# Kernel tuning notes

Hardware: AMD Instinct MI355X
Metric: run time of the kernel (lower is better)

## Reference

```python
import jax, jax.numpy as jnp
import numpy as np

B, W, C, H = 2, 2048, 1024, 16
K = C // H  # 64
LN_EPS = 1e-5


def setup_inputs() -> dict:
    key = jax.random.key(0)
    ks = jax.random.split(key, 8)
    return {
        "seq1": jax.random.normal(ks[0], (B, W, C), jnp.float32),
        "seq2": jax.random.normal(ks[1], (B, W, C), jnp.float32),
        "ln_gamma": jnp.ones((C,), jnp.float32),
        "ln_beta": jnp.zeros((C,), jnp.float32),
        "q_proj": jax.random.normal(ks[2], (H, C, K), jnp.float32) * 0.02,
        "k_proj": jax.random.normal(ks[3], (H, C, K), jnp.float32) * 0.02,
        "v_proj": jax.random.normal(ks[4], (H, C, K), jnp.float32) * 0.02,
        "mixer_w": jax.random.normal(ks[5], (C, C), jnp.float32) * 0.02,
        "mixer_b": jnp.zeros((C,), jnp.float32),
    }


def _layernorm(x, gamma, beta):
    mu = jnp.mean(x, axis=-1, keepdims=True)
    var = jnp.mean(jnp.square(x - mu), axis=-1, keepdims=True)
    return (x - mu) * jax.lax.rsqrt(var + LN_EPS) * gamma + beta


def reference(seq1, seq2, ln_gamma, ln_beta, q_proj, k_proj, v_proj, mixer_w, mixer_b):
    x1 = _layernorm(seq1, ln_gamma, ln_beta)  # [B,W,C]
    x2 = _layernorm(seq2, ln_gamma, ln_beta)
    # per-head projections: [B,W,C] x [H,C,K] -> [B,H,W,K]
    q = jnp.einsum("bwc,hck->bhwk", x1, q_proj)
    k = jnp.einsum("bwc,hck->bhwk", x2, k_proj)
    v = jnp.einsum("bwc,hck->bhwk", x2, v_proj)
    scores = jnp.einsum("bhqk,bhmk->bhqm", q, k) / jnp.sqrt(jnp.float32(K))
    # causal mask (is_decoder=True)
    causal = jnp.tril(jnp.ones((W, W), bool))
    scores = jnp.where(causal[None, None], scores, jnp.float32(-jnp.inf))
    probs = jax.nn.softmax(scores, axis=-1)
    out = jnp.einsum("bhqm,bhmk->bhqk", probs, v)  # [B,H,W,K]
    out = out.transpose(0, 2, 1, 3).reshape(B, W, C)  # [B,W,C]
    return out @ mixer_w.T + mixer_b
```

## Files before the change

### kernel.cpp

```cpp
#include <hip/hip_runtime.h>
#include <math.h>

#define B_ 2
#define W_ 2048
#define C_ 1024
#define H_ 16
#define K_ 64
#define LN_EPS 1e-5f

typedef __attribute__((ext_vector_type(8))) short short8;
typedef __attribute__((ext_vector_type(4))) float float4v;

#if __has_builtin(__builtin_amdgcn_exp2f)
#define EXP2(x) __builtin_amdgcn_exp2f(x)
#else
#define EXP2(x) exp2f(x)
#endif

__device__ inline unsigned short f2bf(float f) {
  unsigned u = __float_as_uint(f);
  u += 0x7fffu + ((u >> 16) & 1u);
  return (unsigned short)(u >> 16);
}

__device__ inline float max3f(float a, float b, float c) {
  return fmaxf(fmaxf(a, b), c);
}

__device__ __forceinline__ void gload_lds16(const short* g, short* l) {
  __builtin_amdgcn_global_load_lds(
      (const __attribute__((address_space(1))) void*)g,
      (__attribute__((address_space(3))) void*)l, 16, 0, 0);
}

__device__ inline float block_sum(float val) {
  __shared__ float sb[4];
  #pragma unroll
  for (int o = 32; o > 0; o >>= 1) val += __shfl_down(val, o, 64);
  int lane = threadIdx.x & 63, wid = threadIdx.x >> 6;
  if (lane == 0) sb[wid] = val;
  __syncthreads();
  float r = sb[0] + sb[1] + sb[2] + sb[3];
  __syncthreads();
  return r;
}

__global__ __launch_bounds__(256) void ln_kernel(
    const float* __restrict__ seq1, const float* __restrict__ seq2,
    const float* __restrict__ gamma, const float* __restrict__ beta,
    short* __restrict__ x1b, short* __restrict__ x2b) {
  int row = blockIdx.x;
  const int nrows = B_ * W_;
  bool first = row < nrows;
  const float* src = first ? seq1 : seq2;
  short* dst = first ? x1b : x2b;
  int r = first ? row : row - nrows;

  const float4* p = (const float4*)(src + (size_t)r * C_);
  float4 v = p[threadIdx.x];
  float mean = block_sum(v.x + v.y + v.z + v.w) * (1.0f / C_);
  float dx = v.x - mean, dy = v.y - mean, dz = v.z - mean, dw = v.w - mean;
  float var = block_sum(dx * dx + dy * dy + dz * dz + dw * dw) * (1.0f / C_);
  float rstd = rsqrtf(var + LN_EPS);

  float4 g = ((const float4*)gamma)[threadIdx.x];
  float4 b = ((const float4*)beta)[threadIdx.x];
  uint2 o;
  o.x = (unsigned)f2bf(dx * rstd * g.x + b.x) |
        ((unsigned)f2bf(dy * rstd * g.y + b.y) << 16);
  o.y = (unsigned)f2bf(dz * rstd * g.z + b.z) |
        ((unsigned)f2bf(dw * rstd * g.w + b.w) << 16);
  ((uint2*)(dst + (size_t)r * C_))[threadIdx.x] = o;
}

__global__ __launch_bounds__(256) void wprep_proj_kernel(
    const float* __restrict__ qp, const float* __restrict__ kp,
    const float* __restrict__ vp,
    short* __restrict__ wqt, short* __restrict__ wkt, short* __restrict__ wvt) {
  int cb = blockIdx.x, h = blockIdx.y, which = blockIdx.z;
  const float* P = (which == 0 ? qp : (which == 1 ? kp : vp)) + (size_t)h * C_ * K_;
  short* Wt = (which == 0 ? wqt : (which == 1 ? wkt : wvt));
  float scale = (which == 0) ? 0.125f * 1.4426950408889634f : 1.0f;

  __shared__ float Ls[64][65];
  int t = threadIdx.x;
  {
    int cr = t >> 2, ks = (t & 3) * 16;
    const float* src = P + (size_t)(cb * 64 + cr) * K_ + ks;
    #pragma unroll
    for (int j = 0; j < 4; ++j) {
      float4 v = *(const float4*)(src + j * 4);
      Ls[cr][ks + j * 4 + 0] = v.x; Ls[cr][ks + j * 4 + 1] = v.y;
      Ls[cr][ks + j * 4 + 2] = v.z; Ls[cr][ks + j * 4 + 3] = v.w;
    }
  }
  __syncthreads();
  int kr = t >> 2, cs = (t & 3) * 16;
  unsigned u[8];
  #pragma unroll
  for (int i = 0; i < 8; ++i) {
    float a = Ls[cs + 2 * i][kr] * scale;
    float b = Ls[cs + 2 * i + 1][kr] * scale;
    u[i] = (unsigned)f2bf(a) | ((unsigned)f2bf(b) << 16);
  }
  short* dst = Wt + ((size_t)h * 64 + kr) * C_ + cb * 64 + cs;
  uint4 p0; p0.x = u[0]; p0.y = u[1]; p0.z = u[2]; p0.w = u[3];
  uint4 p1; p1.x = u[4]; p1.y = u[5]; p1.z = u[6]; p1.w = u[7];
  *(uint4*)dst = p0;
  *(uint4*)(dst + 8) = p1;
}

__global__ __launch_bounds__(256) void wprep_mix_kernel(
    const float* __restrict__ wm, short* __restrict__ wmb) {
  int gid = blockIdx.x * 256 + threadIdx.x;
  float4 v = ((const float4*)wm)[gid];
  uint2 o;
  o.x = (unsigned)f2bf(v.x) | ((unsigned)f2bf(v.y) << 16);
  o.y = (unsigned)f2bf(v.z) | ((unsigned)f2bf(v.w) << 16);
  ((uint2*)wmb)[gid] = o;
}

__device__ __forceinline__ void gemm_core(
    const short* __restrict__ A, const short* __restrict__ Bt,
    int arow0, int brow0, short* As, short* Bs, float4v acc[4][4]) {
  int tid = threadIdx.x;
  int wave = tid >> 6, lane = tid & 63;
  int lr = lane >> 3, lc = lane & 7;
  int sc = lc ^ lr;
  int wr = wave >> 1, wc = wave & 1;
  int lg = lane >> 4, ll = lane & 15;

  #pragma unroll
  for (int mi = 0; mi < 4; ++mi)
    #pragma unroll
    for (int ni = 0; ni < 4; ++ni) {
      acc[mi][ni][0] = 0.f; acc[mi][ni][1] = 0.f;
      acc[mi][ni][2] = 0.f; acc[mi][ni][3] = 0.f;
    }

  for (int k0 = 0; k0 < C_; k0 += 64) {
    __syncthreads();
    #pragma unroll
    for (int j = 0; j < 4; ++j) {
      int seg = wave * 4 + j;
      int r = seg * 8 + lr;
      gload_lds16(A + (size_t)(arow0 + r) * C_ + k0 + sc * 8, As + seg * 512);
      gload_lds16(Bt + (size_t)(brow0 + r) * C_ + k0 + sc * 8, Bs + seg * 512);
    }
    __syncthreads();
    #pragma unroll
    for (int kc = 0; kc < 2; ++kc) {
      int cc = kc * 4 + lg;
      short8 af[4], bf[4];
      #pragma unroll
      for (int mi = 0; mi < 4; ++mi) {
        int m = wr * 64 + mi * 16 + ll;
        af[mi] = *(const short8*)&As[m * 64 + ((cc ^ (m & 7)) << 3)];
      }
      #pragma unroll
      for (int ni = 0; ni < 4; ++ni) {
        int n = wc * 64 + ni * 16 + ll;
        bf[ni] = *(const short8*)&Bs[n * 64 + ((cc ^ (n & 7)) << 3)];
      }
      #pragma unroll
      for (int mi = 0; mi < 4; ++mi)
        #pragma unroll
        for (int ni = 0; ni < 4; ++ni)
          acc[mi][ni] = __builtin_amdgcn_mfma_f32_16x16x32_bf16(
              af[mi], bf[ni], acc[mi][ni], 0, 0, 0);
    }
  }
}

__device__ __forceinline__ void gemm_core64(
    const short* __restrict__ A, const short* __restrict__ Bt,
    int arow0, int brow0, short* As, short* Bs, float4v acc[2][4]) {
  int tid = threadIdx.x;
  int wave = tid >> 6, lane = tid & 63;
  int lr = lane >> 3, lc = lane & 7;
  int sc = lc ^ lr;
  int wr = wave >> 1, wc = wave & 1;
  int lg = lane >> 4, ll = lane & 15;

  #pragma unroll
  for (int mi = 0; mi < 2; ++mi)
    #pragma unroll
    for (int ni = 0; ni < 4; ++ni) {
      acc[mi][ni][0] = 0.f; acc[mi][ni][1] = 0.f;
      acc[mi][ni][2] = 0.f; acc[mi][ni][3] = 0.f;
    }

  for (int k0 = 0; k0 < C_; k0 += 64) {
    __syncthreads();
    #pragma unroll
    for (int j = 0; j < 2; ++j) {
      int seg = wave * 2 + j;
      int r = seg * 8 + lr;
      gload_lds16(A + (size_t)(arow0 + r) * C_ + k0 + sc * 8, As + seg * 512);
    }
    #pragma unroll
    for (int j = 0; j < 4; ++j) {
      int seg = wave * 4 + j;
      int r = seg * 8 + lr;
      gload_lds16(Bt + (size_t)(brow0 + r) * C_ + k0 + sc * 8, Bs + seg * 512);
    }
    __syncthreads();
    #pragma unroll
    for (int kc = 0; kc < 2; ++kc) {
      int cc = kc * 4 + lg;
      short8 af[2], bf[4];
      #pragma unroll
      for (int mi = 0; mi < 2; ++mi) {
        int m = wr * 32 + mi * 16 + ll;
        af[mi] = *(const short8*)&As[m * 64 + ((cc ^ (m & 7)) << 3)];
      }
      #pragma unroll
      for (int ni = 0; ni < 4; ++ni) {
        int n = wc * 64 + ni * 16 + ll;
        bf[ni] = *(const short8*)&Bs[n * 64 + ((cc ^ (n & 7)) << 3)];
      }
      #pragma unroll
      for (int mi = 0; mi < 2; ++mi)
        #pragma unroll
        for (int ni = 0; ni < 4; ++ni)
          acc[mi][ni] = __builtin_amdgcn_mfma_f32_16x16x32_bf16(
              af[mi], bf[ni], acc[mi][ni], 0, 0, 0);
    }
  }
}

__global__ __launch_bounds__(256, 3) void gemm_qkv_kernel(
    const short* __restrict__ x1b, const short* __restrict__ x2b,
    const short* __restrict__ wqt, const short* __restrict__ wkt,
    const short* __restrict__ wvt,
    short* __restrict__ qb, short* __restrict__ kb, short* __restrict__ vtb) {
  __shared__ short As[128 * 64], Bs[128 * 64];
  int z = blockIdx.z;
  const short *A, *Bt;
  int arow0, brow0;
  if (z == 0)      { A = x1b; Bt = wqt; arow0 = blockIdx.x * 128; brow0 = blockIdx.y * 128; }
  else if (z == 1) { A = x2b; Bt = wkt; arow0 = blockIdx.x * 128; brow0 = blockIdx.y * 128; }
  else             { A = wvt; Bt = x2b; arow0 = blockIdx.y * 128; brow0 = blockIdx.x * 128; }

  float4v acc[4][4];
  gemm_core(A, Bt, arow0, brow0, As, Bs, acc);

  int wave = threadIdx.x >> 6, lane = threadIdx.x & 63;
  int wr = wave >> 1, wc = wave & 1, lg = lane >> 4, ll = lane & 15;
  if (z <= 1) {
    short* O = (z == 0) ? qb : kb;
    #pragma unroll
    for (int mi = 0; mi < 4; ++mi)
      #pragma unroll
      for (int ni = 0; ni < 4; ++ni) {
        int n = brow0 + wc * 64 + ni * 16 + ll;
        int h = n >> 6, kk = n & 63;
        #pragma unroll
        for (int r2 = 0; r2 < 4; ++r2) {
          int m = arow0 + wr * 64 + mi * 16 + lg * 4 + r2;
          int b = m >> 11, w = m & (W_ - 1);
          O[((size_t)(b * H_ + h) * W_ + w) * K_ + kk] = (short)f2bf(acc[mi][ni][r2]);
        }
      }
  } else {
    #pragma unroll
    for (int mi = 0; mi < 4; ++mi)
      #pragma unroll
      for (int ni = 0; ni < 4; ++ni) {
        int n = brow0 + wc * 64 + ni * 16 + ll;
        int b = n >> 11, w = n & (W_ - 1);
        #pragma unroll
        for (int r2 = 0; r2 < 4; ++r2) {
          int m = arow0 + wr * 64 + mi * 16 + lg * 4 + r2;
          int h = m >> 6, kk = m & 63;
          vtb[((size_t)(b * H_ + h) * K_ + kk) * W_ + w] = (short)f2bf(acc[mi][ni][r2]);
        }
      }
  }
}

__global__ __launch_bounds__(256, 3) void gemm_mix_kernel(
    const short* __restrict__ attnb, const short* __restrict__ wmb,
    const float* __restrict__ bias, float* __restrict__ out) {
  __shared__ short As[64 * 64], Bs[128 * 64];
  int arow0 = blockIdx.x * 64, brow0 = blockIdx.y * 128;
  float4v acc[2][4];
  gemm_core64(attnb, wmb, arow0, brow0, As, Bs, acc);

  int wave = threadIdx.x >> 6, lane = threadIdx.x & 63;
  int wr = wave >> 1, wc = wave & 1, lg = lane >> 4, ll = lane & 15;
  #pragma unroll
  for (int mi = 0; mi < 2; ++mi)
    #pragma unroll
    for (int ni = 0; ni < 4; ++ni) {
      int n = brow0 + wc * 64 + ni * 16 + ll;
      float bv = bias[n];
      #pragma unroll
      for (int r2 = 0; r2 < 4; ++r2) {
        int m = arow0 + wr * 32 + mi * 16 + lg * 4 + r2;
        out[(size_t)m * C_ + n] = acc[mi][ni][r2] + bv;
      }
    }
}

__global__ __launch_bounds__(256, 3) void attn_mfma_kernel(
    const short* __restrict__ q, const short* __restrict__ k,
    const short* __restrict__ vt, short* __restrict__ out) {
  int bh = blockIdx.x;
  int b = bh >> 4, h = bh & 15;
  int s = blockIdx.y;
  int qt = (s < 16) ? (31 - s) : (s - 16);
  int wave = threadIdx.x >> 6;
  int lane = threadIdx.x & 63;
  int lg = lane >> 4, ll = lane & 15;

  __shared__ short Ks[2][64 * 64];
  __shared__ short Vs[2][64 * 64];
  __shared__ short Ps[4][16 * 72];

  const short* qp = q + (size_t)bh * W_ * K_;
  const short* kp = k + (size_t)bh * W_ * K_;
  const short* vb = vt + (size_t)bh * K_ * W_;

  int qrow = qt * 64 + wave * 16 + ll;
  short8 aq[2];
  #pragma unroll
  for (int kc = 0; kc < 2; ++kc)
    aq[kc] = *(const short8*)(qp + (size_t)qrow * K_ + kc * 32 + lg * 8);

  short8 ones;
  #pragma unroll
  for (int i = 0; i < 8; ++i) ones[i] = (short)0x3F80;

  float4v o[4];
  #pragma unroll
  for (int ct = 0; ct < 4; ++ct) {
    o[ct][0] = 0.f; o[ct][1] = 0.f; o[ct][2] = 0.f; o[ct][3] = 0.f;
  }
  float4v lsum;
  lsum[0] = 0.f; lsum[1] = 0.f; lsum[2] = 0.f; lsum[3] = 0.f;
  float m = -INFINITY;

  int nkt = qt + 1;

  #define STAGE(kt, buf)                                                   \
    {                                                                      \
      const short* kbase = kp + (size_t)(kt) * 64 * K_;                    \
      const short* vbase = vb + (kt) * 64;                                 \
      _Pragma("unroll")                                                    \
      for (int j = 0; j < 2; ++j) {                                        \
        int sdx = j * 256 + (int)threadIdx.x;                              \
        int mm = sdx >> 3, c7 = sdx & 7;                                   \
        int gc = c7 ^ (mm & 7);                                            \
        gload_lds16(kbase + (size_t)mm * K_ + gc * 8, &Ks[buf][sdx * 8]);  \
        gload_lds16(vbase + (size_t)mm * W_ + gc * 8, &Vs[buf][sdx * 8]);  \
      }                                                                    \
    }

  STAGE(0, 0);
  for (int kt = 0; kt < nkt; ++kt) {
    int cur = kt & 1;
    if (kt + 1 < nkt) {
      STAGE(kt + 1, cur ^ 1);
      asm volatile("s_waitcnt vmcnt(4)\ns_barrier" ::: "memory");
    } else {
      asm volatile("s_waitcnt vmcnt(0)\ns_barrier" ::: "memory");
    }

    float4v st[4];
    __builtin_amdgcn_s_setprio(1);
    #pragma unroll
    for (int nt = 0; nt < 4; ++nt) {
      st[nt][0] = 0.f; st[nt][1] = 0.f; st[nt][2] = 0.f; st[nt][3] = 0.f;
      int n = nt * 16 + ll;
      #pragma unroll
      for (int kc = 0; kc < 2; ++kc) {
        int cc = kc * 4 + lg;
        short8 bk = *(const short8*)&Ks[cur][n * 64 + ((cc ^ (n & 7)) << 3)];
        st[nt] = __builtin_amdgcn_mfma_f32_16x16x32_bf16(bk, aq[kc], st[nt], 0, 0, 0);
      }
    }
    __builtin_amdgcn_s_setprio(0);

    short8 bv[4][2];
    #pragma unroll
    for (int ct = 0; ct < 4; ++ct) {
      int c = ct * 16 + ll;
      #pragma unroll
      for (int kc = 0; kc < 2; ++kc) {
        int cc = kc * 4 + lg;
        bv[ct][kc] = *(const short8*)&Vs[cur][c * 64 + ((cc ^ (c & 7)) << 3)];
      }
    }

    if (kt == qt) {
      #pragma unroll
      for (int nt = 0; nt < 4; ++nt) {
        int keyb = nt * 16 + lg * 4;
        #pragma unroll
        for (int r = 0; r < 4; ++r)
          if (keyb + r > wave * 16 + ll) st[nt][r] = -INFINITY;
      }
    }

    float ma = max3f(st[0][0], st[0][1], st[0][2]);
    float mb = max3f(st[0][3], st[1][0], st[1][1]);
    float mc = max3f(st[1][2], st[1][3], st[2][0]);
    float md = max3f(st[2][1], st[2][2], st[2][3]);
    float me = max3f(st[3][0], st[3][1], st[3][2]);
    float lm = fmaxf(max3f(ma, mb, mc), max3f(md, me, st[3][3]));
    lm = fmaxf(lm, __shfl_xor(lm, 16, 64));
    lm = fmaxf(lm, __shfl_xor(lm, 32, 64));
    if (!__all(lm <= m + 8.f)) {
      float nm = fmaxf(m, lm);
      float al = EXP2(m - nm);
      m = nm;
      lsum[0] *= al; lsum[1] *= al; lsum[2] *= al; lsum[3] *= al;
      #pragma unroll
      for (int ct = 0; ct < 4; ++ct) {
        o[ct][0] *= al; o[ct][1] *= al; o[ct][2] *= al; o[ct][3] *= al;
      }
    }

    float p[4][4];
    #pragma unroll
    for (int nt = 0; nt < 4; ++nt)
      #pragma unroll
      for (int r = 0; r < 4; ++r)
        p[nt][r] = EXP2(st[nt][r] - m);

    short* myP = &Ps[wave][ll * 72];
    #pragma unroll
    for (int nt = 0; nt < 4; ++nt) {
      uint2 w;
      w.x = (unsigned)f2bf(p[nt][0]) | ((unsigned)f2bf(p[nt][1]) << 16);
      w.y = (unsigned)f2bf(p[nt][2]) | ((unsigned)f2bf(p[nt][3]) << 16);
      *(uint2*)(myP + nt * 16 + lg * 4) = w;
    }
    __builtin_amdgcn_s_waitcnt(0xC07F);
    short8 bp0 = *(const short8*)(myP + lg * 8);
    short8 bp1 = *(const short8*)(myP + 32 + lg * 8);

    __builtin_amdgcn_s_setprio(1);
    lsum = __builtin_amdgcn_mfma_f32_16x16x32_bf16(ones, bp0, lsum, 0, 0, 0);
    lsum = __builtin_amdgcn_mfma_f32_16x16x32_bf16(ones, bp1, lsum, 0, 0, 0);
    #pragma unroll
    for (int ct = 0; ct < 4; ++ct) {
      o[ct] = __builtin_amdgcn_mfma_f32_16x16x32_bf16(bv[ct][0], bp0, o[ct], 0, 0, 0);
      o[ct] = __builtin_amdgcn_mfma_f32_16x16x32_bf16(bv[ct][1], bp1, o[ct], 0, 0, 0);
    }
    __builtin_amdgcn_s_setprio(0);
    asm volatile("s_waitcnt lgkmcnt(0)\ns_barrier" ::: "memory");
  }
  #undef STAGE

  float invl = 1.0f / lsum[0];
  size_t orow = ((size_t)(b * W_ + qrow)) * C_ + h * K_;
  #pragma unroll
  for (int ct = 0; ct < 4; ++ct) {
    uint2 w;
    w.x = (unsigned)f2bf(o[ct][0] * invl) | ((unsigned)f2bf(o[ct][1] * invl) << 16);
    w.y = (unsigned)f2bf(o[ct][2] * invl) | ((unsigned)f2bf(o[ct][3] * invl) << 16);
    *(uint2*)(out + orow + ct * 16 + lg * 4) = w;
  }
}

extern "C" void kernel_launch(void* const* d_in, const int* in_sizes, int n_in,
                              void* d_out, int out_size, void* d_ws, size_t ws_size,
                              hipStream_t stream) {
  const float* seq1  = (const float*)d_in[0];
  const float* seq2  = (const float*)d_in[1];
  const float* gamma = (const float*)d_in[2];
  const float* beta  = (const float*)d_in[3];
  const float* qp    = (const float*)d_in[4];
  const float* kp    = (const float*)d_in[5];
  const float* vp    = (const float*)d_in[6];
  const float* wm    = (const float*)d_in[7];
  const float* mb    = (const float*)d_in[8];
  float* out = (float*)d_out;

  char* ws = (char*)d_ws;
  const size_t NROW = (size_t)B_ * W_;
  const size_t XB = NROW * C_ * sizeof(short);
  const size_t WB = (size_t)C_ * C_ * sizeof(short);
  short* x1b = (short*)(ws);
  short* x2b = (short*)(ws + XB);
  short* qb  = (short*)(ws + 2 * XB);
  short* kb  = (short*)(ws + 3 * XB);
  short* vtb = (short*)(ws + 4 * XB);
  short* wqt = (short*)(ws + 5 * XB);
  short* wkt = (short*)(ws + 5 * XB + WB);
  short* wvt = (short*)(ws + 5 * XB + 2 * WB);
  short* wmb = (short*)(ws + 5 * XB + 3 * WB);
  short* attnb = (short*)(ws + 5 * XB + 4 * WB);

  wprep_proj_kernel<<<dim3(C_ / 64, H_, 3), dim3(256), 0, stream>>>(
      qp, kp, vp, wqt, wkt, wvt);
  wprep_mix_kernel<<<dim3(C_ * C_ / 1024), dim3(256), 0, stream>>>(wm, wmb);
  ln_kernel<<<dim3(2 * (unsigned)NROW), dim3(256), 0, stream>>>(
      seq1, seq2, gamma, beta, x1b, x2b);
  gemm_qkv_kernel<<<dim3(32, 8, 3), dim3(256), 0, stream>>>(
      x1b, x2b, wqt, wkt, wvt, qb, kb, vtb);
  attn_mfma_kernel<<<dim3(32, 32), dim3(256), 0, stream>>>(
      qb, kb, vtb, attnb);
  gemm_mix_kernel<<<dim3(64, 8), dim3(256), 0, stream>>>(attnb, wmb, mb, out);
}
```

Before: 197.6 us.

## Process two query tiles per attention block to reuse staged K/V tiles

Each attention workgroup now handles 128 query rows as two 64-row tiles (A and B) that share every K/V tile staged in LDS. This halves K/V global loads and staging barriers per query row. The grid shrinks to 512 blocks, launch bounds drop to 2 blocks per CU to allow the doubled accumulator registers, and the causal load-balancing pairing of query tiles is kept. The costs are lower occupancy and fewer blocks, which may leave CUs underused.

After: 219.1 us. 10.9% more time.

```diff
diff --git a/kernel.cpp b/kernel.cpp
--- a/kernel.cpp
+++ b/kernel.cpp
@@ -303,13 +303,13 @@
     }
 }
 
-__global__ __launch_bounds__(256, 3) void attn_mfma_kernel(
+__global__ __launch_bounds__(256, 2) void attn_mfma_kernel(
     const short* __restrict__ q, const short* __restrict__ k,
     const short* __restrict__ vt, short* __restrict__ out) {
   int bh = blockIdx.x;
   int b = bh >> 4, h = bh & 15;
   int s = blockIdx.y;
-  int qt = (s < 16) ? (31 - s) : (s - 16);
+  int qt = (s < 8) ? (15 - s) : (s - 8);
   int wave = threadIdx.x >> 6;
   int lane = threadIdx.x & 63;
   int lg = lane >> 4, ll = lane & 15;
@@ -322,26 +322,31 @@
   const short* kp = k + (size_t)bh * W_ * K_;
   const short* vb = vt + (size_t)bh * K_ * W_;
 
-  int qrow = qt * 64 + wave * 16 + ll;
-  short8 aq[2];
-  #pragma unroll
-  for (int kc = 0; kc < 2; ++kc)
-    aq[kc] = *(const short8*)(qp + (size_t)qrow * K_ + kc * 32 + lg * 8);
+  int qrowA = qt * 128 + wave * 16 + ll;
+  int qrowB = qrowA + 64;
+  short8 aqA[2], aqB[2];
+  #pragma unroll
+  for (int kc = 0; kc < 2; ++kc) {
+    aqA[kc] = *(const short8*)(qp + (size_t)qrowA * K_ + kc * 32 + lg * 8);
+    aqB[kc] = *(const short8*)(qp + (size_t)qrowB * K_ + kc * 32 + lg * 8);
+  }
 
   short8 ones;
   #pragma unroll
   for (int i = 0; i < 8; ++i) ones[i] = (short)0x3F80;
 
-  float4v o[4];
+  float4v oA[4], oB[4];
   #pragma unroll
   for (int ct = 0; ct < 4; ++ct) {
-    o[ct][0] = 0.f; o[ct][1] = 0.f; o[ct][2] = 0.f; o[ct][3] = 0.f;
-  }
-  float4v lsum;
-  lsum[0] = 0.f; lsum[1] = 0.f; lsum[2] = 0.f; lsum[3] = 0.f;
-  float m = -INFINITY;
-
-  int nkt = qt + 1;
+    oA[ct][0] = 0.f; oA[ct][1] = 0.f; oA[ct][2] = 0.f; oA[ct][3] = 0.f;
+    oB[ct][0] = 0.f; oB[ct][1] = 0.f; oB[ct][2] = 0.f; oB[ct][3] = 0.f;
+  }
+  float4v lsA, lsB;
+  lsA[0] = 0.f; lsA[1] = 0.f; lsA[2] = 0.f; lsA[3] = 0.f;
+  lsB[0] = 0.f; lsB[1] = 0.f; lsB[2] = 0.f; lsB[3] = 0.f;
+  float mA = -INFINITY, mB = -INFINITY;
+
+  int nkt = 2 * qt + 2;
 
   #define STAGE(kt, buf)                                                   \
     {                                                                      \
@@ -367,17 +372,35 @@
       asm volatile("s_waitcnt vmcnt(0)\ns_barrier" ::: "memory");
     }
 
-    float4v st[4];
+    bool haveA = (kt <= 2 * qt);
+
+    float4v stA[4], stB[4];
     __builtin_amdgcn_s_setprio(1);
-    #pragma unroll
-    for (int nt = 0; nt < 4; ++nt) {
-      st[nt][0] = 0.f; st[nt][1] = 0.f; st[nt][2] = 0.f; st[nt][3] = 0.f;
-      int n = nt * 16 + ll;
-      #pragma unroll
-      for (int kc = 0; kc < 2; ++kc) {
-        int cc = kc * 4 + lg;
-        short8 bk = *(const short8*)&Ks[cur][n * 64 + ((cc ^ (n & 7)) << 3)];
-        st[nt] = __builtin_amdgcn_mfma_f32_16x16x32_bf16(bk, aq[kc], st[nt], 0, 0, 0);
+    if (haveA) {
+      #pragma unroll
+      for (int nt = 0; nt < 4; ++nt) {
+        stA[nt][0] = 0.f; stA[nt][1] = 0.f; stA[nt][2] = 0.f; stA[nt][3] = 0.f;
+        stB[nt][0] = 0.f; stB[nt][1] = 0.f; stB[nt][2] = 0.f; stB[nt][3] = 0.f;
+        int n = nt * 16 + ll;
+        #pragma unroll
+        for (int kc = 0; kc < 2; ++kc) {
+          int cc = kc * 4 + lg;
+          short8 bk = *(const short8*)&Ks[cur][n * 64 + ((cc ^ (n & 7)) << 3)];
+          stA[nt] = __builtin_amdgcn_mfma_f32_16x16x32_bf16(bk, aqA[kc], stA[nt], 0, 0, 0);
+          stB[nt] = __builtin_amdgcn_mfma_f32_16x16x32_bf16(bk, aqB[kc], stB[nt], 0, 0, 0);
+        }
+      }
+    } else {
+      #pragma unroll
+      for (int nt = 0; nt < 4; ++nt) {
+        stB[nt][0] = 0.f; stB[nt][1] = 0.f; stB[nt][2] = 0.f; stB[nt][3] = 0.f;
+        int n = nt * 16 + ll;
+        #pragma unroll
+        for (int kc = 0; kc < 2; ++kc) {
+          int cc = kc * 4 + lg;
+          short8 bk = *(const short8*)&Ks[cur][n * 64 + ((cc ^ (n & 7)) << 3)];
+          stB[nt] = __builtin_amdgcn_mfma_f32_16x16x32_bf16(bk, aqB[kc], stB[nt], 0, 0, 0);
+        }
       }
     }
     __builtin_amdgcn_s_setprio(0);
@@ -393,75 +416,144 @@
       }
     }
 
-    if (kt == qt) {
+    if (kt == 2 * qt) {
       #pragma unroll
       for (int nt = 0; nt < 4; ++nt) {
         int keyb = nt * 16 + lg * 4;
         #pragma unroll
         for (int r = 0; r < 4; ++r)
-          if (keyb + r > wave * 16 + ll) st[nt][r] = -INFINITY;
-      }
-    }
-
-    float ma = max3f(st[0][0], st[0][1], st[0][2]);
-    float mb = max3f(st[0][3], st[1][0], st[1][1]);
-    float mc = max3f(st[1][2], st[1][3], st[2][0]);
-    float md = max3f(st[2][1], st[2][2], st[2][3]);
-    float me = max3f(st[3][0], st[3][1], st[3][2]);
-    float lm = fmaxf(max3f(ma, mb, mc), max3f(md, me, st[3][3]));
-    lm = fmaxf(lm, __shfl_xor(lm, 16, 64));
-    lm = fmaxf(lm, __shfl_xor(lm, 32, 64));
-    if (!__all(lm <= m + 8.f)) {
-      float nm = fmaxf(m, lm);
-      float al = EXP2(m - nm);
-      m = nm;
-      lsum[0] *= al; lsum[1] *= al; lsum[2] *= al; lsum[3] *= al;
+          if (keyb + r > wave * 16 + ll) stA[nt][r] = -INFINITY;
+      }
+    }
+    if (kt == 2 * qt + 1) {
+      #pragma unroll
+      for (int nt = 0; nt < 4; ++nt) {
+        int keyb = nt * 16 + lg * 4;
+        #pragma unroll
+        for (int r = 0; r < 4; ++r)
+          if (keyb + r > wave * 16 + ll) stB[nt][r] = -INFINITY;
+      }
+    }
+
+    short* myP = &Ps[wave][ll * 72];
+
+    if (haveA) {
+      float ma = max3f(stA[0][0], stA[0][1], stA[0][2]);
+      float mb2 = max3f(stA[0][3], stA[1][0], stA[1][1]);
+      float mc = max3f(stA[1][2], stA[1][3], stA[2][0]);
+      float md = max3f(stA[2][1], stA[2][2], stA[2][3]);
+      float me = max3f(stA[3][0], stA[3][1], stA[3][2]);
+      float lm = fmaxf(max3f(ma, mb2, mc), max3f(md, me, stA[3][3]));
+      lm = fmaxf(lm, __shfl_xor(lm, 16, 64));
+      lm = fmaxf(lm, __shfl_xor(lm, 32, 64));
+      if (!__all(lm <= mA + 8.f)) {
+        float nm = fmaxf(mA, lm);
+        float al = EXP2(mA - nm);
+        mA = nm;
+        lsA[0] *= al; lsA[1] *= al; lsA[2] *= al; lsA[3] *= al;
+        #pragma unroll
+        for (int ct = 0; ct < 4; ++ct) {
+          oA[ct][0] *= al; oA[ct][1] *= al; oA[ct][2] *= al; oA[ct][3] *= al;
+        }
+      }
+      float p[4][4];
+      #pragma unroll
+      for (int nt = 0; nt < 4; ++nt)
+        #pragma unroll
+        for (int r = 0; r < 4; ++r)
+          p[nt][r] = EXP2(stA[nt][r] - mA);
+      #pragma unroll
+      for (int nt = 0; nt < 4; ++nt) {
+        uint2 w;
+        w.x = (unsigned)f2bf(p[nt][0]) | ((unsigned)f2bf(p[nt][1]) << 16);
+        w.y = (unsigned)f2bf(p[nt][2]) | ((unsigned)f2bf(p[nt][3]) << 16);
+        *(uint2*)(myP + nt * 16 + lg * 4) = w;
+      }
+      __builtin_amdgcn_s_waitcnt(0xC07F);
+      short8 bp0 = *(const short8*)(myP + lg * 8);
+      short8 bp1 = *(const short8*)(myP + 32 + lg * 8);
+      __builtin_amdgcn_s_setprio(1);
+      lsA = __builtin_amdgcn_mfma_f32_16x16x32_bf16(ones, bp0, lsA, 0, 0, 0);
+      lsA = __builtin_amdgcn_mfma_f32_16x16x32_bf16(ones, bp1, lsA, 0, 0, 0);
       #pragma unroll
       for (int ct = 0; ct < 4; ++ct) {
-        o[ct][0] *= al; o[ct][1] *= al; o[ct][2] *= al; o[ct][3] *= al;
-      }
-    }
-
-    float p[4][4];
-    #pragma unroll
-    for (int nt = 0; nt < 4; ++nt)
-      #pragma unroll
-      for (int r = 0; r < 4; ++r)
-        p[nt][r] = EXP2(st[nt][r] - m);
-
-    short* myP = &Ps[wave][ll * 72];
-    #pragma unroll
-    for (int nt = 0; nt < 4; ++nt) {
+        oA[ct] = __builtin_amdgcn_mfma_f32_16x16x32_bf16(bv[ct][0], bp0, oA[ct], 0, 0, 0);
+        oA[ct] = __builtin_amdgcn_mfma_f32_16x16x32_bf16(bv[ct][1], bp1, oA[ct], 0, 0, 0);
+      }
+      __builtin_amdgcn_s_setprio(0);
+    }
+
+    {
+      float ma = max3f(stB[0][0], stB[0][1], stB[0][2]);
+      float mb2 = max3f(stB[0][3], stB[1][0], stB[1][1]);
+      float mc = max3f(stB[1][2], stB[1][3], stB[2][0]);
+      float md = max3f(stB[2][1], stB[2][2], stB[2][3]);
+      float me = max3f(stB[3][0], stB[3][1], stB[3][2]);
+      float lm = fmaxf(max3f(ma, mb2, mc), max3f(md, me, stB[3][3]));
+      lm = fmaxf(lm, __shfl_xor(lm, 16, 64));
+      lm = fmaxf(lm, __shfl_xor(lm, 32, 64));
+      if (!__all(lm <= mB + 8.f)) {
+        float nm = fmaxf(mB, lm);
+        float al = EXP2(mB - nm);
+        mB = nm;
+        lsB[0] *= al; lsB[1] *= al; lsB[2] *= al; lsB[3] *= al;
+        #pragma unroll
+        for (int ct = 0; ct < 4; ++ct) {
+          oB[ct][0] *= al; oB[ct][1] *= al; oB[ct][2] *= al; oB[ct][3] *= al;
+        }
+      }
+      float p[4][4];
+      #pragma unroll
+      for (int nt = 0; nt < 4; ++nt)
+        #pragma unroll
+        for (int r = 0; r < 4; ++r)
+          p[nt][r] = EXP2(stB[nt][r] - mB);
+      #pragma unroll
+      for (int nt = 0; nt < 4; ++nt) {
+        uint2 w;
+        w.x = (unsigned)f2bf(p[nt][0]) | ((unsigned)f2bf(p[nt][1]) << 16);
+        w.y = (unsigned)f2bf(p[nt][2]) | ((unsigned)f2bf(p[nt][3]) << 16);
+        *(uint2*)(myP + nt * 16 + lg * 4) = w;
+      }
+      __builtin_amdgcn_s_waitcnt(0xC07F);
+      short8 bp0 = *(const short8*)(myP + lg * 8);
+      short8 bp1 = *(const short8*)(myP + 32 + lg * 8);
+      __builtin_amdgcn_s_setprio(1);
+      lsB = __builtin_amdgcn_mfma_f32_16x16x32_bf16(ones, bp0, lsB, 0, 0, 0);
+      lsB = __builtin_amdgcn_mfma_f32_16x16x32_bf16(ones, bp1, lsB, 0, 0, 0);
+      #pragma unroll
+      for (int ct = 0; ct < 4; ++ct) {
+        oB[ct] = __builtin_amdgcn_mfma_f32_16x16x32_bf16(bv[ct][0], bp0, oB[ct], 0, 0, 0);
+        oB[ct] = __builtin_amdgcn_mfma_f32_16x16x32_bf16(bv[ct][1], bp1, oB[ct], 0, 0, 0);
+      }
+      __builtin_amdgcn_s_setprio(0);
+    }
+
+    asm volatile("s_waitcnt lgkmcnt(0)\ns_barrier" ::: "memory");
+  }
+  #undef STAGE
+
+  {
+    float invl = 1.0f / lsA[0];
+    size_t orow = ((size_t)(b * W_ + qrowA)) * C_ + h * K_;
+    #pragma unroll
+    for (int ct = 0; ct < 4; ++ct) {
       uint2 w;
-      w.x = (unsigned)f2bf(p[nt][0]) | ((unsigned)f2bf(p[nt][1]) << 16);
-      w.y = (unsigned)f2bf(p[nt][2]) | ((unsigned)f2bf(p[nt][3]) << 16);
-      *(uint2*)(myP + nt * 16 + lg * 4) = w;
-    }
-    __builtin_amdgcn_s_waitcnt(0xC07F);
-    short8 bp0 = *(const short8*)(myP + lg * 8);
-    short8 bp1 = *(const short8*)(myP + 32 + lg * 8);
-
-    __builtin_amdgcn_s_setprio(1);
-    lsum = __builtin_amdgcn_mfma_f32_16x16x32_bf16(ones, bp0, lsum, 0, 0, 0);
-    lsum = __builtin_amdgcn_mfma_f32_16x16x32_bf16(ones, bp1, lsum, 0, 0, 0);
+      w.x = (unsigned)f2bf(oA[ct][0] * invl) | ((unsigned)f2bf(oA[ct][1] * invl) << 16);
+      w.y = (unsigned)f2bf(oA[ct][2] * invl) | ((unsigned)f2bf(oA[ct][3] * invl) << 16);
+      *(uint2*)(out + orow + ct * 16 + lg * 4) = w;
+    }
+  }
+  {
+    float invl = 1.0f / lsB[0];
+    size_t orow = ((size_t)(b * W_ + qrowB)) * C_ + h * K_;
     #pragma unroll
     for (int ct = 0; ct < 4; ++ct) {
-      o[ct] = __builtin_amdgcn_mfma_f32_16x16x32_bf16(bv[ct][0], bp0, o[ct], 0, 0, 0);
-      o[ct] = __builtin_amdgcn_mfma_f32_16x16x32_bf16(bv[ct][1], bp1, o[ct], 0, 0, 0);
-    }
-    __builtin_amdgcn_s_setprio(0);
-    asm volatile("s_waitcnt lgkmcnt(0)\ns_barrier" ::: "memory");
-  }
-  #undef STAGE
-
-  float invl = 1.0f / lsum[0];
-  size_t orow = ((size_t)(b * W_ + qrow)) * C_ + h * K_;
-  #pragma unroll
-  for (int ct = 0; ct < 4; ++ct) {
-    uint2 w;
-    w.x = (unsigned)f2bf(o[ct][0] * invl) | ((unsigned)f2bf(o[ct][1] * invl) << 16);
-    w.y = (unsigned)f2bf(o[ct][2] * invl) | ((unsigned)f2bf(o[ct][3] * invl) << 16);
-    *(uint2*)(out + orow + ct * 16 + lg * 4) = w;
+      uint2 w;
+      w.x = (unsigned)f2bf(oB[ct][0] * invl) | ((unsigned)f2bf(oB[ct][1] * invl) << 16);
+      w.y = (unsigned)f2bf(oB[ct][2] * invl) | ((unsigned)f2bf(oB[ct][3] * invl) << 16);
+      *(uint2*)(out + orow + ct * 16 + lg * 4) = w;
+    }
   }
 }
 
@@ -501,7 +593,7 @@
       seq1, seq2, gamma, beta, x1b, x2b);
   gemm_qkv_kernel<<<dim3(32, 8, 3), dim3(256), 0, stream>>>(
       x1b, x2b, wqt, wkt, wvt, qb, kb, vtb);
-  attn_mfma_kernel<<<dim3(32, 32), dim3(256), 0, stream>>>(
+  attn_mfma_kernel<<<dim3(32, 16), dim3(256), 0, stream>>>(
       qb, kb, vtb, attnb);
   gemm_mix_kernel<<<dim3(64, 8), dim3(256), 0, stream>>>(attnb, wmb, mb, out);
 }
```
